# Kernel optimization log

Hardware: AMD Instinct MI355X
Metric: run time of the kernel (lower is better)

Reference implementation:

```python
import jax, jax.numpy as jnp
import numpy as np


def setup_inputs() -> dict:
    key = jax.random.key(0)
    ks = jax.random.split(key, 8)
    B, C, H, W = 16, 192, 64, 64
    dt_rank, d_state = 12, 1
    return {
        "x": jax.random.normal(ks[0], (B, C, H, W), dtype=jnp.float32),
        "conv_w": jax.random.normal(ks[1], (C, 1, 5, 5), dtype=jnp.float32) * 0.1,
        "conv_b": jax.random.normal(ks[2], (C,), dtype=jnp.float32) * 0.1,
        "x_proj_w": jax.random.normal(ks[3], (dt_rank + 2 * d_state, C), dtype=jnp.float32) * (C ** -0.5),
        "dt_w": jax.random.normal(ks[4], (C, dt_rank), dtype=jnp.float32) * (dt_rank ** -0.5),
        "dt_b": jax.random.normal(ks[5], (C,), dtype=jnp.float32) * 0.1,
        "A_logs": jnp.zeros((C, d_state), dtype=jnp.float32),  # log(arange(1,d_state+1)) with d_state=1 -> 0
        "Ds": jnp.ones((C,), dtype=jnp.float32),
    }


def reference(x, conv_w, conv_b, x_proj_w, dt_w, dt_b, A_logs, Ds):
    B, C, H, W = x.shape
    L = H * W
    dt_rank = dt_w.shape[1]
    n = A_logs.shape[1]  # d_state
    # depthwise conv2d, kernel 5, padding SAME (=d_conv//2), then SiLU
    x = jax.lax.conv_general_dilated(
        x, conv_w, window_strides=(1, 1), padding='SAME',
        feature_group_count=C, dimension_numbers=('NCHW', 'OIHW', 'NCHW'))
    x = jax.nn.silu(x + conv_b[None, :, None, None])
    xs = x.reshape(B, C, L)  # (b, d, l)
    # x_proj: (dt_rank + 2n, C) @ (b, C, l)
    x_dbl = jnp.einsum('kc,bcl->bkl', x_proj_w, xs)
    dts, Bs, Cs = jnp.split(x_dbl, [dt_rank, dt_rank + n], axis=1)
    # dt projection + softplus (delta_softplus=True with delta_bias)
    delta = jax.nn.softplus(jnp.einsum('cr,brl->bcl', dt_w, dts) + dt_b[None, :, None])  # (b,d,l)
    A = -jnp.exp(A_logs)  # (d, n)
    # selective scan returning the full state trajectory h_t (b,d,n,l):
    # h_t = exp(delta_t * A) * h_{t-1} + delta_t * B_t * u_t
    a = jnp.exp(delta[:, :, None, :] * A[None, :, :, None])        # (b,d,n,l)
    b_el = delta[:, :, None, :] * Bs[:, None, :, :] * xs[:, :, None, :]  # (b,d,n,l)

    def combine(e1, e2):
        a1, b1 = e1
        a2, b2 = e2
        return (a1 * a2, a2 * b1 + b2)

    _, h = jax.lax.associative_scan(combine, (a, b_el), axis=-1)  # h: (b,d,n,l)
    state = h.reshape(B, C * n, L)
    # y = C_t * h_t + D * u (fp32, d_state=1 broadcast)
    y = state.astype(jnp.float32) * Cs.astype(jnp.float32) + xs * Ds[:, None]
    return y.reshape(B, C, H, W)
```

## Files before the change

### kernel.cpp

```cpp
#include <hip/hip_runtime.h>
#include <hip/hip_bf16.h>
#include <cstddef>

#define BB 16
#define CC 192
#define HH 64
#define WW 64
#define LL 4096
#define DTR 12
#define KK 14

__device__ __forceinline__ float silu_f(float v) {
  return v / (1.f + __expf(-v));
}

__global__ __launch_bounds__(256) void conv_silu_kernel(
    const float* __restrict__ x, const float* __restrict__ cw,
    const float* __restrict__ cb, float* __restrict__ xs) {
  const int bc = blockIdx.x;
  const int c = bc % CC;
  const int tid = threadIdx.x;
  const int lane = tid & 63;
  const int wv = tid >> 6;
  const int oy0 = wv * 16;

  float w[25];
#pragma unroll
  for (int k = 0; k < 25; ++k) w[k] = cw[c * 25 + k];
  const float bias = cb[c];

  const float* xp = x + (size_t)bc * LL + lane;
  float* op = xs + (size_t)bc * LL + lane;

  float acc[5];
#pragma unroll
  for (int i = 0; i < 5; ++i) acc[i] = 0.f;

#pragma unroll 5
  for (int r = 0; r < 20; ++r) {
    const int gr = oy0 + r - 2;
    float v = 0.f;
    if ((unsigned)gr < 64u) v = xp[gr * 64];
    float vm2 = __shfl_up(v, 2u, 64);
    float vm1 = __shfl_up(v, 1u, 64);
    float vp1 = __shfl_down(v, 1u, 64);
    float vp2 = __shfl_down(v, 2u, 64);
    if (lane < 2) vm2 = 0.f;
    if (lane < 1) vm1 = 0.f;
    if (lane > 62) vp1 = 0.f;
    if (lane > 61) vp2 = 0.f;
    float t[5] = {vm2, vm1, v, vp1, vp2};
#pragma unroll
    for (int ky = 0; ky < 5; ++ky) {
      if (r >= ky && (r - ky) < 16) {
        float s = acc[(r - ky) % 5];
#pragma unroll
        for (int kx = 0; kx < 5; ++kx) s += w[ky * 5 + kx] * t[kx];
        acc[(r - ky) % 5] = s;
      }
    }
    if (r >= 4) {
      const int yf = oy0 + r - 4;
      float a = acc[(r - 4) % 5] + bias;
      op[yf * 64] = silu_f(a);
      acc[(r - 4) % 5] = 0.f;
    }
  }
}

__global__ __launch_bounds__(512) void proj_kernel(
    const float* __restrict__ xs, const float* __restrict__ xpw,
    float* __restrict__ xdbl) {
  const int b = blockIdx.y;
  const int l0 = blockIdx.x * 128;
  const int tid = threadIdx.x;
  const int lane = tid & 63;
  const int g = tid >> 6;

  __shared__ float part[8][KK][132];

  float2 acc[KK];
#pragma unroll
  for (int k = 0; k < KK; ++k) acc[k] = make_float2(0.f, 0.f);

  const float* bp = xs + ((size_t)(b * CC + g * 24)) * LL + l0 + lane * 2;
#pragma unroll 4
  for (int cc = 0; cc < 24; ++cc) {
    float2 v = *(const float2*)(bp + (size_t)cc * LL);
    const int c = g * 24 + cc;
#pragma unroll
    for (int k = 0; k < KK; ++k) {
      float wv = xpw[k * CC + c];
      acc[k].x += wv * v.x;
      acc[k].y += wv * v.y;
    }
  }
#pragma unroll
  for (int k = 0; k < KK; ++k)
    *(float2*)&part[g][k][lane * 2] = acc[k];
  __syncthreads();

  for (int idx = tid; idx < KK * 128; idx += 512) {
    int k = idx >> 7, ln = idx & 127;
    float v = 0.f;
#pragma unroll
    for (int p = 0; p < 8; ++p) v += part[p][k][ln];
    xdbl[((size_t)b * KK + k) * LL + l0 + ln] = v;
  }
}

__global__ __launch_bounds__(64) void scan_kernel(
    const float* __restrict__ xs, const float* __restrict__ xdbl,
    const float* __restrict__ dtw, const float* __restrict__ dtb,
    const float* __restrict__ A_logs, const float* __restrict__ Ds,
    float* __restrict__ y) {
  const int bc = blockIdx.x;
  const int b = bc / CC;
  const int c = bc - b * CC;
  const int lane = threadIdx.x;

  const float Ac = -__expf(A_logs[c]);
  const float Dc = Ds[c];
  float dw[DTR];
#pragma unroll
  for (int r = 0; r < DTR; ++r) dw[r] = dtw[c * DTR + r];
  const float db = dtb[c];

  const float* xp = xs + (size_t)bc * LL;
  const float* xb = xdbl + (size_t)b * KK * LL;
  float* yp = y + (size_t)bc * LL;

  float hcarry = 0.f;

  for (int sc = 0; sc < 16; ++sc) {
    const int base = sc * 256 + lane * 4;

    float4 x4 = *(const float4*)(xp + base);
    float4 B4 = *(const float4*)(xb + 12 * LL + base);
    float4 C4 = *(const float4*)(xb + 13 * LL + base);
    float4 dr[DTR];
#pragma unroll
    for (int r = 0; r < DTR; ++r)
      dr[r] = *(const float4*)(xb + r * LL + base);

    float xx[4] = {x4.x, x4.y, x4.z, x4.w};
    float bb[4] = {B4.x, B4.y, B4.z, B4.w};
    float av[4], bv[4];
    float aggA = 1.f, aggB = 0.f;
#pragma unroll
    for (int q = 0; q < 4; ++q) {
      float z = db;
#pragma unroll
      for (int r = 0; r < DTR; ++r) z += dw[r] * ((&dr[r].x)[q]);
      float delta = (z > 15.f) ? z : __logf(1.f + __expf(z));
      float a = __expf(delta * Ac);
      float be = delta * bb[q] * xx[q];
      av[q] = a;
      bv[q] = be;
      aggA = a * aggA;
      aggB = a * aggB + be;
    }

    float incA = aggA, incB = aggB;
#pragma unroll
    for (int s = 1; s < 64; s <<= 1) {
      float pA = __shfl_up(incA, (unsigned)s, 64);
      float pB = __shfl_up(incB, (unsigned)s, 64);
      if (lane >= s) {
        incB = incA * pB + incB;
        incA = incA * pA;
      }
    }
    float eA = __shfl_up(incA, 1u, 64);
    float eB = __shfl_up(incB, 1u, 64);
    if (lane == 0) { eA = 1.f; eB = 0.f; }
    float tA = __shfl(incA, 63, 64);
    float tB = __shfl(incB, 63, 64);

    float h = eA * hcarry + eB;
    float ov[4];
#pragma unroll
    for (int q = 0; q < 4; ++q) {
      h = av[q] * h + bv[q];
      ov[q] = h * ((&C4.x)[q]) + xx[q] * Dc;
    }
    float4 o;
    o.x = ov[0]; o.y = ov[1]; o.z = ov[2]; o.w = ov[3];
    *(float4*)(yp + base) = o;

    hcarry = tA * hcarry + tB;
  }
}

extern "C" void kernel_launch(void* const* d_in, const int* in_sizes, int n_in,
                              void* d_out, int out_size, void* d_ws,
                              size_t ws_size, hipStream_t stream) {
  const float* x        = (const float*)d_in[0];
  const float* conv_w   = (const float*)d_in[1];
  const float* conv_b   = (const float*)d_in[2];
  const float* x_proj_w = (const float*)d_in[3];
  const float* dt_w     = (const float*)d_in[4];
  const float* dt_b     = (const float*)d_in[5];
  const float* A_logs   = (const float*)d_in[6];
  const float* Ds       = (const float*)d_in[7];
  float* out = (float*)d_out;

  char* ws = (char*)d_ws;
  const size_t plane_bytes = (size_t)BB * CC * LL * sizeof(float);
  float* xs   = (float*)ws;
  float* xdbl = (float*)(ws + plane_bytes);

  conv_silu_kernel<<<dim3(BB * CC), 256, 0, stream>>>(x, conv_w, conv_b, xs);
  proj_kernel<<<dim3(LL / 128, BB), 512, 0, stream>>>(xs, x_proj_w, xdbl);
  scan_kernel<<<dim3(BB * CC), 64, 0, stream>>>(xs, xdbl, dt_w, dt_b,
                                                A_logs, Ds, out);
}
```

Before: 187.7 us.

## Software-pipeline scan chunk loads and batch conv row loads upfront

The scan kernel now double-buffers its per-chunk loads, prefetching the next 256-element chunk of xs and xdbl into registers while the current chunk is processed. This is meant to hide global memory latency in the serial 16-iteration loop. The conv kernel loads all 20 input rows into registers before computing, so more loads are in flight at once. Both changes raise register pressure, and the last iteration redundantly reloads chunk 15.

```diff
diff --git a/kernel.cpp b/kernel.cpp
--- a/kernel.cpp
+++ b/kernel.cpp
@@ -32,15 +32,22 @@
   const float* xp = x + (size_t)bc * LL + lane;
   float* op = xs + (size_t)bc * LL + lane;
 
-  float acc[5];
-#pragma unroll
-  for (int i = 0; i < 5; ++i) acc[i] = 0.f;
-
-#pragma unroll 5
+  float rv[20];
+#pragma unroll
   for (int r = 0; r < 20; ++r) {
     const int gr = oy0 + r - 2;
     float v = 0.f;
     if ((unsigned)gr < 64u) v = xp[gr * 64];
+    rv[r] = v;
+  }
+
+  float acc[5];
+#pragma unroll
+  for (int i = 0; i < 5; ++i) acc[i] = 0.f;
+
+#pragma unroll
+  for (int r = 0; r < 20; ++r) {
+    float v = rv[r];
     float vm2 = __shfl_up(v, 2u, 64);
     float vm1 = __shfl_up(v, 1u, 64);
     float vp1 = __shfl_down(v, 1u, 64);
@@ -132,17 +139,21 @@
 
   float hcarry = 0.f;
 
-  for (int sc = 0; sc < 16; ++sc) {
+  auto load_chunk = [&](int sc, float4* dst) {
     const int base = sc * 256 + lane * 4;
-
-    float4 x4 = *(const float4*)(xp + base);
-    float4 B4 = *(const float4*)(xb + 12 * LL + base);
-    float4 C4 = *(const float4*)(xb + 13 * LL + base);
-    float4 dr[DTR];
+    dst[0] = *(const float4*)(xp + base);
+    dst[1] = *(const float4*)(xb + 12 * LL + base);
+    dst[2] = *(const float4*)(xb + 13 * LL + base);
 #pragma unroll
     for (int r = 0; r < DTR; ++r)
-      dr[r] = *(const float4*)(xb + r * LL + base);
-
+      dst[3 + r] = *(const float4*)(xb + r * LL + base);
+  };
+
+  auto process = [&](int sc, const float4* buf) {
+    const int base = sc * 256 + lane * 4;
+    const float4 x4 = buf[0];
+    const float4 B4 = buf[1];
+    const float4 C4 = buf[2];
     float xx[4] = {x4.x, x4.y, x4.z, x4.w};
     float bb[4] = {B4.x, B4.y, B4.z, B4.w};
     float av[4], bv[4];
@@ -151,7 +162,7 @@
     for (int q = 0; q < 4; ++q) {
       float z = db;
 #pragma unroll
-      for (int r = 0; r < DTR; ++r) z += dw[r] * ((&dr[r].x)[q]);
+      for (int r = 0; r < DTR; ++r) z += dw[r] * ((&buf[3 + r].x)[q]);
       float delta = (z > 15.f) ? z : __logf(1.f + __expf(z));
       float a = __expf(delta * Ac);
       float be = delta * bb[q] * xx[q];
@@ -189,6 +200,16 @@
     *(float4*)(yp + base) = o;
 
     hcarry = tA * hcarry + tB;
+  };
+
+  float4 bufA[15], bufB[15];
+  load_chunk(0, bufA);
+  for (int i = 0; i < 8; ++i) {
+    const int s0 = 2 * i;
+    load_chunk(s0 + 1, bufB);
+    process(s0, bufA);
+    load_chunk(s0 + 2 < 16 ? s0 + 2 : 15, bufA);
+    process(s0 + 1, bufB);
   }
 }
 
```

After: 171.9 us. 8.4% less time.
